# Performance work log

Measured on AMD Instinct MI355X. Metric: run time of the kernel, lower is better.

The kernel has to match this reference:

```python
import jax, jax.numpy as jnp
import numpy as np

B, E, L = 8, 512, 8192
MAX_W = 4          # max_subword_block_width -> widths 1..3
KSIZE = 5          # conv_kernel_size
DS = 2             # downsample_rate


def setup_inputs() -> dict:
    key = jax.random.key(0)
    k0, k1, k2, k3 = jax.random.split(key, 4)
    x = jax.random.normal(k0, (B, E, L), dtype=jnp.float32)
    # Conv1d(E, E, KSIZE): weight [out_ch, in_ch, k], bias [out_ch]
    conv_w = jax.random.normal(k1, (E, E, KSIZE), dtype=jnp.float32) * (1.0 / np.sqrt(E * KSIZE))
    conv_b = jax.random.normal(k2, (E,), dtype=jnp.float32) * 0.01
    # Linear(E, 1, bias=False): stored as vector [E]
    score_w = jax.random.normal(k3, (E,), dtype=jnp.float32) * (1.0 / np.sqrt(E))
    return {"x": x, "conv_w": conv_w, "conv_b": conv_b, "score_w": score_w}


def reference(x, conv_w, conv_b, score_w):
    length = x.shape[-1]  # original length, captured BEFORE the valid conv (as in torch)
    # Pre-GBST conv, VALID padding -> length shrinks by KSIZE-1
    y = jax.lax.conv_general_dilated(
        x, conv_w, window_strides=(1,), padding="VALID",
        dimension_numbers=("NCH", "OIH", "NCH"))
    y = y + conv_b[None, :, None]

    seqs, scs = [], []
    for w in range(1, MAX_W):
        Lc = y.shape[-1]
        pad = (-Lc) % w
        yp = jnp.pad(y, ((0, 0), (0, 0), (0, pad))) if pad else y
        # avg_pool1d(kernel=w, stride=w) == reshape + mean (zero-pad counts in mean, matching torch)
        cand = yp.reshape(yp.shape[0], yp.shape[1], -1, w).mean(-1)  # [B,E,Nb]
        sc = jnp.einsum("ben,e->bn", cand, score_w)                  # [B,Nb]
        rs = jnp.repeat(cand, w, axis=-1)  # [B,E,Nb*w]
        rc = jnp.repeat(sc, w, axis=-1)    # [B,Nb*w]
        Lr = rs.shape[-1]
        if Lr < length:
            rs = jnp.pad(rs, ((0, 0), (0, 0), (0, length - Lr)))
            rc = jnp.pad(rc, ((0, 0), (0, length - Lr)))
        seqs.append(rs[:, :, :length])
        scs.append(rc[:, :length])
    seqs = jnp.stack(seqs, axis=-1)            # [B,E,L,W-1]
    scs = jnp.stack(scs, axis=-1)[:, None]     # [B,1,L,W-1]
    att = jax.nn.softmax(scs, axis=-1)
    out = (seqs * att).sum(-1)                 # [B,E,L]
    # Downsample via avg_pool1d(kernel=DS, stride=DS)
    b, e, l = out.shape
    out = out[:, :, :(l // DS) * DS].reshape(b, e, l // DS, DS).mean(-1)
    return out
```

## Files before the change

kernel.cpp:

```cpp
#include <hip/hip_runtime.h>
#include <math.h>

#define B_    8
#define E_    512
#define L_    8192
#define K_    5
#define LC    8188
#define LOUT  4096
#define LPAD  8256

typedef float  f32x4   __attribute__((ext_vector_type(4)));
typedef float  f32x16  __attribute__((ext_vector_type(16)));
typedef short  s16x4   __attribute__((ext_vector_type(4)));
typedef short  s16x8   __attribute__((ext_vector_type(8)));

__device__ __forceinline__ unsigned short f2bf(float f) {
    union { float f; unsigned u; } v; v.f = f;
    unsigned r = v.u + 0x7FFFu + ((v.u >> 16) & 1u);
    return (unsigned short)(r >> 16);
}
__device__ __forceinline__ float bf2f(unsigned short h) {
    union { unsigned u; float f; } v; v.u = ((unsigned)h) << 16;
    return v.f;
}

__global__ __launch_bounds__(256) void wt_kernel(const float* __restrict__ w,
                                                 unsigned short* __restrict__ Wtb) {
    int idx = blockIdx.x * 256 + threadIdx.x;
    if (idx >= E_ * E_ * K_) return;
    int i    = idx & (E_ - 1);
    int rest = idx >> 9;
    int e    = rest & (E_ - 1);
    int k    = rest >> 9;
    Wtb[idx] = f2bf(w[((size_t)e * E_ + i) * K_ + k]);
}

__global__ __launch_bounds__(256) void xt_kernel(const float* __restrict__ x,
                                                 unsigned short* __restrict__ xT) {
    __shared__ float s[64][65];
    const int b  = blockIdx.z;
    const int i0 = blockIdx.y * 64;
    const int t0 = blockIdx.x * 64;
    #pragma unroll
    for (int j = 0; j < 16; ++j) {
        int idx = threadIdx.x + j * 256;
        int r = idx >> 6, c = idx & 63;
        int t = t0 + c;
        s[c][r] = (t < L_) ? x[((size_t)b * E_ + i0 + r) * L_ + t] : 0.f;
    }
    __syncthreads();
    #pragma unroll
    for (int j = 0; j < 4; ++j) {
        int idx = threadIdx.x + j * 256;
        int tt = idx >> 4, ig = (idx & 15) * 4;
        s16x4 v;
        v[0] = (short)f2bf(s[tt][ig + 0]);
        v[1] = (short)f2bf(s[tt][ig + 1]);
        v[2] = (short)f2bf(s[tt][ig + 2]);
        v[3] = (short)f2bf(s[tt][ig + 3]);
        *(s16x4*)&xT[((size_t)b * LPAD + t0 + tt) * E_ + i0 + ig] = v;
    }
}

__global__ __launch_bounds__(256) void zero_z(float* __restrict__ z) {
    int idx = blockIdx.x * 256 + threadIdx.x;
    if (idx < (B_ * LC) / 4) ((f32x4*)z)[idx] = (f32x4)0.f;
}

__global__ __launch_bounds__(256, 2) void conv_mfma(const unsigned short* __restrict__ xT,
                                                    const unsigned short* __restrict__ Wtb,
                                                    const float* __restrict__ bias,
                                                    const float* __restrict__ sw,
                                                    unsigned short* __restrict__ y,
                                                    float* __restrict__ z) {
    __shared__ unsigned short Xs[520][40];
    __shared__ unsigned short Ws[K_][64][40];
    __shared__ float swb[128];

    const int tid  = threadIdx.x;
    const int nt   = blockIdx.x;
    const int b    = nt >> 4;
    const int tb   = (nt & 15) * 512;
    const int e0   = blockIdx.y * 64;
    const int wave = tid >> 6;
    const int lane = tid & 63;
    const int l32  = lane & 31;
    const int hi   = lane >> 5;
    const int wt0  = wave * 128;

    if (tid < 64)       swb[tid] = sw[e0 + tid];
    else if (tid < 128) swb[tid] = bias[e0 + tid - 64];

    f32x16 acc[2][4];
    #pragma unroll
    for (int es = 0; es < 2; ++es)
        #pragma unroll
        for (int ts = 0; ts < 4; ++ts) acc[es][ts] = (f32x16)0.f;

    const unsigned short* xbase = xT + ((size_t)b * LPAD + tb) * E_;

    s16x8 xpf[9];
    s16x8 wpf[5];

    auto load_tile = [&](int i0) {
        #pragma unroll
        for (int j = 0; j < 8; ++j) {
            int idx = tid + j * 256;
            int r = idx >> 2, c = idx & 3;
            xpf[j] = *(const s16x8*)(xbase + (size_t)r * E_ + i0 + c * 8);
        }
        {
            int idx = tid + 2048;
            if (idx < 2080) {
                int r = idx >> 2, c = idx & 3;
                xpf[8] = *(const s16x8*)(xbase + (size_t)r * E_ + i0 + c * 8);
            }
        }
        #pragma unroll
        for (int j = 0; j < 5; ++j) {
            int idx = tid + j * 256;
            int rl = idx >> 2, c = idx & 3;
            int k = rl >> 6, ep = rl & 63;
            wpf[j] = *(const s16x8*)(Wtb + ((size_t)(k * E_ + e0 + ep) * E_ + i0 + c * 8));
        }
    };
    auto store_tile = [&]() {
        #pragma unroll
        for (int j = 0; j < 8; ++j) {
            int idx = tid + j * 256;
            int r = idx >> 2, c = idx & 3;
            *(s16x8*)&Xs[r][c * 8] = xpf[j];
        }
        {
            int idx = tid + 2048;
            if (idx < 2080) {
                int r = idx >> 2, c = idx & 3;
                *(s16x8*)&Xs[r][c * 8] = xpf[8];
            }
        }
        #pragma unroll
        for (int j = 0; j < 5; ++j) {
            int idx = tid + j * 256;
            int rl = idx >> 2, c = idx & 3;
            int k = rl >> 6, ep = rl & 63;
            *(s16x8*)&Ws[k][ep][c * 8] = wpf[j];
        }
    };

    load_tile(0);
    for (int i0 = 0; i0 < E_; i0 += 32) {
        __syncthreads();
        store_tile();
        __syncthreads();
        if (i0 + 32 < E_) load_tile(i0 + 32);

        #pragma unroll
        for (int k = 0; k < K_; ++k) {
            #pragma unroll
            for (int kk = 0; kk < 2; ++kk) {
                const int co = kk * 16 + hi * 8;
                s16x8 a0 = *(const s16x8*)&Ws[k][l32][co];
                s16x8 a1 = *(const s16x8*)&Ws[k][32 + l32][co];
                #pragma unroll
                for (int ts = 0; ts < 4; ++ts) {
                    s16x8 bv = *(const s16x8*)&Xs[wt0 + ts * 32 + l32 + k][co];
                    acc[0][ts] = __builtin_amdgcn_mfma_f32_32x32x16_bf16(a0, bv, acc[0][ts], 0, 0, 0);
                    acc[1][ts] = __builtin_amdgcn_mfma_f32_32x32x16_bf16(a1, bv, acc[1][ts], 0, 0, 0);
                }
            }
        }
    }

    #pragma unroll
    for (int ts = 0; ts < 4; ++ts) {
        const int t = tb + wt0 + ts * 32 + l32;
        const bool tv = (t < LC);
        float zp = 0.f;
        #pragma unroll
        for (int es = 0; es < 2; ++es) {
            #pragma unroll
            for (int reg = 0; reg < 16; ++reg) {
                int er = es * 32 + (reg & 3) + 8 * (reg >> 2) + 4 * hi;
                float v = acc[es][ts][reg] + swb[64 + er];
                if (tv) y[((size_t)b * E_ + e0 + er) * LC + t] = f2bf(v);
                zp += swb[er] * v;
            }
        }
        zp += __shfl_xor(zp, 32);
        if (hi == 0 && tv) atomicAdd(&z[(size_t)b * LC + t], zp);
    }
}

#define DTILE 256
#define STAGE 520
__global__ __launch_bounds__(256) void out_kernel(const unsigned short* __restrict__ y,
                                                  const float* __restrict__ z,
                                                  float* __restrict__ out) {
    __shared__ float ys[STAGE];
    __shared__ float zs[STAGE];
    const int be = blockIdx.x;
    const int b  = be >> 9;
    const int d0 = blockIdx.y * DTILE;
    const int tb = d0 * 2;
    const unsigned short* yrow = y + (size_t)be * LC;
    const float* zrow = z + (size_t)b * LC;
    for (int i = threadIdx.x; i < STAGE; i += 256) {
        int t = tb - 2 + i;
        bool v = (t >= 0) && (t < LC);
        ys[i] = v ? bf2f(yrow[t]) : 0.f;
        zs[i] = v ? zrow[t] : 0.f;
    }
    __syncthreads();
    const int d = d0 + threadIdx.x;
    float o = 0.f;
    #pragma unroll
    for (int half = 0; half < 2; ++half) {
        int t = 2 * d + half;
        int j = t - tb + 2;
        float C1 = ys[j], S1 = zs[j];
        int i2 = (t & ~1) - tb + 2;
        float C2 = 0.5f * (ys[i2] + ys[i2 + 1]);
        float S2 = 0.5f * (zs[i2] + zs[i2 + 1]);
        int i3 = (t / 3) * 3 - tb + 2;
        float C3 = (ys[i3] + ys[i3 + 1] + ys[i3 + 2]) * (1.f / 3.f);
        float S3 = (zs[i3] + zs[i3 + 1] + zs[i3 + 2]) * (1.f / 3.f);
        float m  = fmaxf(S1, fmaxf(S2, S3));
        float a1 = __expf(S1 - m), a2 = __expf(S2 - m), a3 = __expf(S3 - m);
        o += (a1 * C1 + a2 * C2 + a3 * C3) / (a1 + a2 + a3);
    }
    out[(size_t)be * LOUT + d] = 0.5f * o;
}

extern "C" void kernel_launch(void* const* d_in, const int* in_sizes, int n_in,
                              void* d_out, int out_size, void* d_ws, size_t ws_size,
                              hipStream_t stream) {
    const float* x       = (const float*)d_in[0];
    const float* conv_w  = (const float*)d_in[1];
    const float* conv_b  = (const float*)d_in[2];
    const float* score_w = (const float*)d_in[3];
    float* out = (float*)d_out;

    unsigned short* base = (unsigned short*)d_ws;
    unsigned short* Wtb = base;
    unsigned short* xT  = Wtb + (size_t)K_ * E_ * E_;
    unsigned short* y   = xT + (size_t)B_ * LPAD * E_;
    float*          z   = (float*)(y + (size_t)B_ * E_ * LC);

    wt_kernel<<<dim3((E_ * E_ * K_ + 255) / 256), 256, 0, stream>>>(conv_w, Wtb);
    xt_kernel<<<dim3(LPAD / 64, E_ / 64, B_), 256, 0, stream>>>(x, xT);
    zero_z<<<dim3((B_ * LC / 4 + 255) / 256), 256, 0, stream>>>(z);
    conv_mfma<<<dim3(B_ * 16, E_ / 64), 256, 0, stream>>>(xT, Wtb, conv_b, score_w, y, z);
    out_kernel<<<dim3(B_ * E_, LOUT / DTILE), 256, 0, stream>>>(y, z, out);
}
```

Baseline: 448.4 us.

## Pad y/z buffers with zero halos and share softmax weights across channels

Result: faster. 419.2 us (-6.5%).

```diff
diff --git a/kernel.cpp b/kernel.cpp
--- a/kernel.cpp
+++ b/kernel.cpp
@@ -7,7 +7,9 @@
 #define K_    5
 #define LC    8188
 #define LOUT  4096
-#define LPAD  8256
+#define XROWS 8200
+#define LCP   8208
+
 
 typedef float  f32x4   __attribute__((ext_vector_type(4)));
 typedef float  f32x16  __attribute__((ext_vector_type(16)));
@@ -19,9 +21,11 @@
     unsigned r = v.u + 0x7FFFu + ((v.u >> 16) & 1u);
     return (unsigned short)(r >> 16);
 }
-__device__ __forceinline__ float bf2f(unsigned short h) {
-    union { unsigned u; float f; } v; v.u = ((unsigned)h) << 16;
-    return v.f;
+__device__ __forceinline__ float bflo(unsigned u) {
+    union { unsigned u; float f; } v; v.u = u << 16; return v.f;
+}
+__device__ __forceinline__ float bfhi(unsigned u) {
+    union { unsigned u; float f; } v; v.u = u & 0xFFFF0000u; return v.f;
 }
 
 __global__ __launch_bounds__(256) void wt_kernel(const float* __restrict__ w,
@@ -58,21 +62,28 @@
         v[1] = (short)f2bf(s[tt][ig + 1]);
         v[2] = (short)f2bf(s[tt][ig + 2]);
         v[3] = (short)f2bf(s[tt][ig + 3]);
-        *(s16x4*)&xT[((size_t)b * LPAD + t0 + tt) * E_ + i0 + ig] = v;
-    }
-}
-
-__global__ __launch_bounds__(256) void zero_z(float* __restrict__ z) {
+        *(s16x4*)&xT[((size_t)b * XROWS + t0 + tt) * E_ + i0 + ig] = v;
+    }
+}
+
+__global__ __launch_bounds__(256) void zero_aux(unsigned short* __restrict__ yP,
+                                                float* __restrict__ zP) {
     int idx = blockIdx.x * 256 + threadIdx.x;
-    if (idx < (B_ * LC) / 4) ((f32x4*)z)[idx] = (f32x4)0.f;
+    if (idx < B_ * LCP) zP[idx] = 0.f;
+    int i2 = idx - B_ * LCP;
+    if (i2 >= 0 && i2 < B_ * E_ * 20) {
+        int row = i2 / 20, j = i2 - row * 20;
+        int col = (j < 8) ? j : (8 + LC + (j - 8));
+        yP[(size_t)row * LCP + col] = 0;
+    }
 }
 
 __global__ __launch_bounds__(256, 2) void conv_mfma(const unsigned short* __restrict__ xT,
                                                     const unsigned short* __restrict__ Wtb,
                                                     const float* __restrict__ bias,
                                                     const float* __restrict__ sw,
-                                                    unsigned short* __restrict__ y,
-                                                    float* __restrict__ z) {
+                                                    unsigned short* __restrict__ yP,
+                                                    float* __restrict__ zP) {
     __shared__ unsigned short Xs[520][40];
     __shared__ unsigned short Ws[K_][64][40];
     __shared__ float swb[128];
@@ -97,7 +108,7 @@
         #pragma unroll
         for (int ts = 0; ts < 4; ++ts) acc[es][ts] = (f32x16)0.f;
 
-    const unsigned short* xbase = xT + ((size_t)b * LPAD + tb) * E_;
+    const unsigned short* xbase = xT + ((size_t)b * XROWS + tb) * E_;
 
     s16x8 xpf[9];
     s16x8 wpf[5];
@@ -182,53 +193,92 @@
             for (int reg = 0; reg < 16; ++reg) {
                 int er = es * 32 + (reg & 3) + 8 * (reg >> 2) + 4 * hi;
                 float v = acc[es][ts][reg] + swb[64 + er];
-                if (tv) y[((size_t)b * E_ + e0 + er) * LC + t] = f2bf(v);
+                if (tv) yP[((size_t)(b * E_ + e0 + er)) * LCP + 8 + t] = f2bf(v);
                 zp += swb[er] * v;
             }
         }
         zp += __shfl_xor(zp, 32);
-        if (hi == 0 && tv) atomicAdd(&z[(size_t)b * LC + t], zp);
-    }
-}
-
-#define DTILE 256
-#define STAGE 520
-__global__ __launch_bounds__(256) void out_kernel(const unsigned short* __restrict__ y,
-                                                  const float* __restrict__ z,
-                                                  float* __restrict__ out) {
-    __shared__ float ys[STAGE];
-    __shared__ float zs[STAGE];
-    const int be = blockIdx.x;
-    const int b  = be >> 9;
-    const int d0 = blockIdx.y * DTILE;
-    const int tb = d0 * 2;
-    const unsigned short* yrow = y + (size_t)be * LC;
-    const float* zrow = z + (size_t)b * LC;
-    for (int i = threadIdx.x; i < STAGE; i += 256) {
-        int t = tb - 2 + i;
-        bool v = (t >= 0) && (t < LC);
-        ys[i] = v ? bf2f(yrow[t]) : 0.f;
-        zs[i] = v ? zrow[t] : 0.f;
-    }
+        if (hi == 0 && tv) atomicAdd(&zP[(size_t)b * LCP + 8 + t], zp);
+    }
+}
+
+__global__ __launch_bounds__(256) void out2_kernel(const unsigned short* __restrict__ yP,
+                                                   const float* __restrict__ zP,
+                                                   float* __restrict__ out) {
+    __shared__ unsigned short ys8[8][1040];
+    __shared__ float  zsL[1040];
+    __shared__ float2 attA[512];
+    __shared__ float2 attB[512];
+    __shared__ float  attC[512];
+    const int bx  = blockIdx.x;
+    const int b   = bx >> 6;
+    const int eg  = bx & 63;
+    const int d0  = blockIdx.y << 9;
+    const int tid = threadIdx.x;
+
+    const unsigned short* ybase = yP + ((size_t)(b * E_ + eg * 8)) * LCP + 2 * d0;
+    const float* zbase = zP + (size_t)b * LCP + 2 * d0;
+
+    #pragma unroll
+    for (int r = 0; r < 8; ++r) {
+        if (tid < 130) {
+            s16x8 v = *(const s16x8*)(ybase + (size_t)r * LCP + tid * 8);
+            *(s16x8*)&ys8[r][tid * 8] = v;
+        }
+    }
+    for (int c = tid; c < 260; c += 256)
+        *(f32x4*)&zsL[c * 4] = *(const f32x4*)(zbase + c * 4);
     __syncthreads();
-    const int d = d0 + threadIdx.x;
-    float o = 0.f;
-    #pragma unroll
-    for (int half = 0; half < 2; ++half) {
-        int t = 2 * d + half;
-        int j = t - tb + 2;
-        float C1 = ys[j], S1 = zs[j];
-        int i2 = (t & ~1) - tb + 2;
-        float C2 = 0.5f * (ys[i2] + ys[i2 + 1]);
-        float S2 = 0.5f * (zs[i2] + zs[i2 + 1]);
-        int i3 = (t / 3) * 3 - tb + 2;
-        float C3 = (ys[i3] + ys[i3 + 1] + ys[i3 + 2]) * (1.f / 3.f);
-        float S3 = (zs[i3] + zs[i3 + 1] + zs[i3 + 2]) * (1.f / 3.f);
-        float m  = fmaxf(S1, fmaxf(S2, S3));
-        float a1 = __expf(S1 - m), a2 = __expf(S2 - m), a3 = __expf(S3 - m);
-        o += (a1 * C1 + a2 * C2 + a3 * C3) / (a1 + a2 + a3);
-    }
-    out[(size_t)be * LOUT + d] = 0.5f * o;
+
+    for (int dl = tid; dl < 512; dl += 256) {
+        int lt = 2 * dl + 6;
+        float z0 = zsL[lt + 0], z1 = zsL[lt + 1], z2 = zsL[lt + 2];
+        float z3 = zsL[lt + 3], z4 = zsL[lt + 4], z5 = zsL[lt + 5];
+        unsigned t  = 2u * (unsigned)(d0 + dl);
+        unsigned r3 = t % 3u;
+        float a12 = z1 + z2, a34 = z3 + z4;
+        float s0 = z0 + a12, s1 = a12 + z3, s2 = z2 + a34, s3 = a34 + z5;
+        float S1a = z2, S1b = z3;
+        float S2  = 0.5f * (z2 + z3);
+        float S3a = ((r3 == 0u) ? s2 : ((r3 == 1u) ? s1 : s0)) * (1.f / 3.f);
+        float S3b = ((r3 == 0u) ? s2 : ((r3 == 1u) ? s1 : s3)) * (1.f / 3.f);
+        float m0 = fmaxf(S1a, fmaxf(S2, S3a));
+        float e1 = __expf(S1a - m0), e2 = __expf(S2 - m0), e3 = __expf(S3a - m0);
+        float r0 = 1.f / (e1 + e2 + e3);
+        float m1 = fmaxf(S1b, fmaxf(S2, S3b));
+        float f1 = __expf(S1b - m1), f2 = __expf(S2 - m1), f3 = __expf(S3b - m1);
+        float r1 = 1.f / (f1 + f2 + f3);
+        attA[dl] = make_float2(0.5f * e1 * r0, 0.5f * f1 * r1);
+        attB[dl] = make_float2(0.25f * (e2 * r0 + f2 * r1), (0.5f / 3.f) * e3 * r0);
+        attC[dl] = (0.5f / 3.f) * f3 * r1;
+    }
+    __syncthreads();
+
+    const int e    = tid >> 5;
+    const int l32b = tid & 31;
+    float* orow = out + ((size_t)(b * E_ + eg * 8 + e)) * LOUT + d0;
+    const unsigned short* yr = &ys8[e][0];
+    #pragma unroll
+    for (int ii = 0; ii < 16; ++ii) {
+        int dl = l32b + 32 * ii;
+        unsigned u0 = *(const unsigned*)(yr + 2 * dl + 6);
+        unsigned u1 = *(const unsigned*)(yr + 2 * dl + 8);
+        unsigned u2 = *(const unsigned*)(yr + 2 * dl + 10);
+        float v0 = bflo(u0), v1 = bfhi(u0);
+        float v2 = bflo(u1), v3 = bfhi(u1);
+        float v4 = bflo(u2), v5 = bfhi(u2);
+        unsigned t  = 2u * (unsigned)(d0 + dl);
+        unsigned r3 = t % 3u;
+        float a12 = v1 + v2, a34 = v3 + v4;
+        float s0 = v0 + a12, s1 = a12 + v3, s2 = v2 + a34, s3 = a34 + v5;
+        float C3a = (r3 == 0u) ? s2 : ((r3 == 1u) ? s1 : s0);
+        float C3b = (r3 == 0u) ? s2 : ((r3 == 1u) ? s1 : s3);
+        float2 wA = attA[dl];
+        float2 wB = attB[dl];
+        float  wC = attC[dl];
+        float o = wA.x * v2 + wA.y * v3 + wB.x * (v2 + v3) + wB.y * C3a + wC * C3b;
+        orow[dl] = o;
+    }
 }
 
 extern "C" void kernel_launch(void* const* d_in, const int* in_sizes, int n_in,
@@ -243,12 +293,12 @@
     unsigned short* base = (unsigned short*)d_ws;
     unsigned short* Wtb = base;
     unsigned short* xT  = Wtb + (size_t)K_ * E_ * E_;
-    unsigned short* y   = xT + (size_t)B_ * LPAD * E_;
-    float*          z   = (float*)(y + (size_t)B_ * E_ * LC);
+    unsigned short* yP  = xT + (size_t)B_ * XROWS * E_;
+    float*          zP  = (float*)(yP + (size_t)B_ * E_ * LCP);
 
     wt_kernel<<<dim3((E_ * E_ * K_ + 255) / 256), 256, 0, stream>>>(conv_w, Wtb);
-    xt_kernel<<<dim3(LPAD / 64, E_ / 64, B_), 256, 0, stream>>>(x, xT);
-    zero_z<<<dim3((B_ * LC / 4 + 255) / 256), 256, 0, stream>>>(z);
-    conv_mfma<<<dim3(B_ * 16, E_ / 64), 256, 0, stream>>>(xT, Wtb, conv_b, score_w, y, z);
-    out_kernel<<<dim3(B_ * E_, LOUT / DTILE), 256, 0, stream>>>(y, z, out);
-}
+    xt_kernel<<<dim3(L_ / 64, E_ / 64, B_), 256, 0, stream>>>(x, xT);
+    zero_aux<<<dim3((B_ * LCP + B_ * E_ * 20 + 255) / 256), 256, 0, stream>>>(yP, zP);
+    conv_mfma<<<dim3(B_ * 16, E_ / 64), 256, 0, stream>>>(xT, Wtb, conv_b, score_w, yP, zP);
+    out2_kernel<<<dim3(B_ * 64, LOUT / 512), 256, 0, stream>>>(yP, zP, out);
+}
```
